# Kernel optimization log

Hardware: AMD Instinct MI355X
Metric: run time of the kernel (lower is better)

Reference implementation:

```python
import jax, jax.numpy as jnp
import numpy as np

NF = 32
B, H, W = 4, 256, 256


def conv(x, w, b, pad):
    y = jax.lax.conv_general_dilated(x, w, (1, 1), [(pad, pad), (pad, pad)],
                                     dimension_numbers=('NCHW', 'OIHW', 'NCHW'))
    return y + b[None, :, None, None]


def maxpool(x):  # kernel 3, stride 2, pad 1 (pad with -inf like torch)
    return jax.lax.reduce_window(x, -jnp.inf, jax.lax.max,
                                 (1, 1, 3, 3), (1, 1, 2, 2),
                                 [(0, 0), (0, 0), (1, 1), (1, 1)])


def up2(x):  # bilinear x2, align_corners=False (half-pixel) == jax.image default
    b, c, h, w = x.shape
    return jax.image.resize(x, (b, c, 2 * h, 2 * w), 'bilinear')


def norm_gates(g1, g2, g3):
    s = jnp.abs(g1) + jnp.abs(g2) + jnp.abs(g3)
    s = jnp.where(s == 0, 1e-6, s)
    m = (s >= 1).astype(g1.dtype)
    return tuple((1 - m) * g + m * (g / s) for g in (g1, g2, g3))


def propagate(x, g1, g2, g3, horizontal, reverse):
    """GateRecurrent2dnoind: sequential gated scan along one spatial axis.
    h[t] = (1 - g1 - g2 - g3) * x[t] + g1*h[t-1](i-1) + g2*h[t-1](i) + g3*h[t-1](i+1)
    with zero boundary for out-of-range neighbors."""
    if not horizontal:
        x, g1, g2, g3 = (jnp.swapaxes(t, 2, 3) for t in (x, g1, g2, g3))
    if reverse:
        x, g1, g2, g3 = (t[..., ::-1] for t in (x, g1, g2, g3))
    seqs = tuple(jnp.moveaxis(t, 3, 0) for t in (x, g1, g2, g3))  # [W,B,C,H]

    def step(h, inp):
        xt, a1, a2, a3 = inp
        z = jnp.zeros_like(h[..., :1])
        h_up = jnp.concatenate([z, h[..., :-1]], axis=-1)   # neighbor i-1
        h_dn = jnp.concatenate([h[..., 1:], z], axis=-1)    # neighbor i+1
        hn = (1 - a1 - a2 - a3) * xt + a1 * h_up + a2 * h + a3 * h_dn
        return hn, hn

    h0 = jnp.zeros(x.shape[:3], x.dtype)
    _, ys = jax.lax.scan(step, h0, seqs)
    out = jnp.moveaxis(ys, 0, 3)
    if reverse:
        out = out[..., ::-1]
    if not horizontal:
        out = jnp.swapaxes(out, 2, 3)
    return out


def spn_forward(x, rgb, mw, mb, c1w, c1b, c2w, c2b, c3w, c3b, c4w, c4b,
                d0w, d0b, d2w, d2b, d4w, d4b, d6w, d6b, d7w, d7b, pw, pb):
    nf = NF
    X = conv(x, mw, mb, 1)
    # VGG encoder
    f1 = conv(rgb, c1w, c1b, 1)
    p = maxpool(jax.nn.relu(f1))
    f2 = conv(p, c2w, c2b, 1)
    p = maxpool(jax.nn.relu(f2))
    f3 = conv(p, c3w, c3b, 1)
    p3 = maxpool(jax.nn.relu(f3))
    f4 = conv(p3, c4w, c4b, 1)
    # Decoder
    o = conv(f4, d0w, d0b, 0)
    o = jax.nn.elu(conv(up2(o), d2w, d2b, 1)) + f3
    o = jax.nn.elu(conv(up2(o), d4w, d4b, 1)) + f2
    o = jax.nn.elu(conv(up2(o), d6w, d6b, 1)) + f1
    guide = conv(o, d7w, d7b, 1)  # [B, 12*nf, H, W]
    G = [guide[:, i * nf:(i + 1) * nf] for i in range(12)]
    dirs = [(True, False), (True, True), (False, False), (False, True)]
    outs = []
    for k, (hor, rev) in enumerate(dirs):
        g1, g2, g3 = norm_gates(G[3 * k], G[3 * k + 1], G[3 * k + 2])
        outs.append(propagate(X, g1, g2, g3, hor, rev))
    out = jnp.maximum(jnp.maximum(outs[0], outs[1]), jnp.maximum(outs[2], outs[3]))
    return conv(out, pw, pb, 1)


def setup_inputs() -> dict:
    key = jax.random.key(0)
    ks = jax.random.split(key, 32)
    nf = NF

    def p(k, shape):
        return jax.random.normal(k, shape, dtype=jnp.float32) * 0.1

    inp = {
        'x': jax.random.normal(ks[0], (B, 3, H, W), dtype=jnp.float32),
        'rgb': jax.random.normal(ks[1], (B, 3, H, W), dtype=jnp.float32),
        'mw': p(ks[2], (nf, 3, 3, 3)), 'mb': p(ks[3], (nf,)),
        'c1w': p(ks[4], (nf, 3, 3, 3)), 'c1b': p(ks[5], (nf,)),
        'c2w': p(ks[6], (nf * 2, nf, 3, 3)), 'c2b': p(ks[7], (nf * 2,)),
        'c3w': p(ks[8], (nf * 4, nf * 2, 3, 3)), 'c3b': p(ks[9], (nf * 4,)),
        'c4w': p(ks[10], (nf * 8, nf * 4, 3, 3)), 'c4b': p(ks[11], (nf * 8,)),
        'd0w': p(ks[12], (nf * 4, nf * 8, 1, 1)), 'd0b': p(ks[13], (nf * 4,)),
        'd2w': p(ks[14], (nf * 4, nf * 4, 3, 3)), 'd2b': p(ks[15], (nf * 4,)),
        'd4w': p(ks[16], (nf * 2, nf * 4, 3, 3)), 'd4b': p(ks[17], (nf * 2,)),
        'd6w': p(ks[18], (nf, nf * 2, 3, 3)), 'd6b': p(ks[19], (nf,)),
        'd7w': p(ks[20], (nf * 12, nf, 3, 3)), 'd7b': p(ks[21], (nf * 12,)),
        'pw': p(ks[22], (3, nf, 3, 3)), 'pb': p(ks[23], (3,)),
    }
    return inp


def reference(x, rgb, mw, mb, c1w, c1b, c2w, c2b, c3w, c3b, c4w, c4b,
              d0w, d0b, d2w, d2b, d4w, d4b, d6w, d6b, d7w, d7b, pw, pb):
    return spn_forward(x, rgb, mw, mb, c1w, c1b, c2w, c2b, c3w, c3b, c4w, c4b,
                       d0w, d0b, d2w, d2b, d4w, d4b, d6w, d6b, d7w, d7b, pw, pb)
```

## Files before the change

### kernel.cpp

```cpp
#include <hip/hip_runtime.h>
#include <cstddef>
#include <cstdint>

#define DEVINL __device__ __forceinline__

typedef __attribute__((ext_vector_type(8))) _Float16 half8v;
typedef __attribute__((ext_vector_type(16))) float f32x16;

constexpr int cmax(int a, int b) { return a > b ? a : b; }


__global__ __launch_bounds__(256) void k_repack(
    const float* __restrict__ src, float* __restrict__ dst, int Cin, int Cout)
{
  int n = Cout * Cin * 9;
  int e = blockIdx.x * 256 + threadIdx.x;
  if (e >= n) return;
  int co = e / (Cin * 9);
  int r  = e - co * Cin * 9;
  int ci = r / 9;
  int k  = r - ci * 9;
  dst[(ci * 9 + k) * Cout + co] = src[e];
}

__global__ __launch_bounds__(256) void k_packwh(
    const float* __restrict__ src, _Float16* __restrict__ dst, int Cin, int Cout)
{
  int chunks = Cin >> 4;
  int total = Cout * chunks * 144;
  int e = blockIdx.x * 256 + threadIdx.x;
  if (e >= total) return;
  int n  = e / (chunks * 144);
  int r2 = e - n * chunks * 144;
  int cb = r2 / 144;
  int k  = r2 - cb * 144;
  int tap = k >> 4, ci = k & 15;
  float v = src[((size_t)n * Cin + cb * 16 + ci) * 9 + tap];
  dst[((size_t)cb * Cout + n) * 152 + k] = (_Float16)v;
}

template<int NWM, int NACC, int CHUNKS, int MODE, int GATES>
__global__ __launch_bounds__(NWM * 64) void k_convh(
    const float* __restrict__ in, const _Float16* __restrict__ wpk,
    const float* __restrict__ bias, const float* __restrict__ skip,
    void* __restrict__ outv,
    int H, int W, int wCout, int n0, int outC, int oco0)
{
  static_assert(GATES == 0 || NACC == 3, "GATES needs NACC==3");
  constexpr int NTHR = NWM * 64;
  constexpr int ROWS = NWM * 2;
  constexpr int RH = ROWS + 2;
  constexpr int N_BLK = NACC * 32;
  constexpr int MT = NWM * 32;
  constexpr int A_BYTES = RH * 18 * 16 * 2;
  constexpr int B_BYTES = N_BLK * 152 * 2;
  constexpr int MPF = MT + 1;
  constexpr int MPH = 132;
  constexpr int EP_BYTES = GATES ? (96 * MPH * 2) : (N_BLK * MPF * 4);
  constexpr int SMEM = cmax(A_BYTES + B_BYTES, EP_BYTES);

  const int tid = threadIdx.x;
  const int wave = tid >> 6, lane = tid & 63;
  const int wm = wave;
  const int tiles_x = W >> 4;
  const int tx0 = (blockIdx.x % tiles_x) << 4;
  const int ty0 = (blockIdx.x / tiles_x) * ROWS;
  const int b = blockIdx.z;
  const int nb = n0 + blockIdx.y * N_BLK;
  const int ocb = oco0 + blockIdx.y * N_BLK;

  __shared__ __align__(16) char smem[SMEM];
  _Float16* Ah = (_Float16*)smem;
  _Float16* Bh = (_Float16*)(smem + A_BYTES);

  f32x16 acc[NACC] = {};

  const size_t ps = (size_t)H * W;
  const float* inb = in + (size_t)b * (CHUNKS * 16) * ps;

  for (int cb = 0; cb < CHUNKS; ++cb) {
    __syncthreads();
    for (int e = tid; e < RH * 18; e += NTHR) {
      int r = e / 18, c = e - r * 18;
      int gy = ty0 + r - 1, gx = tx0 + c - 1;
      bool ok = (unsigned)gy < (unsigned)H && (unsigned)gx < (unsigned)W;
      const float* src = inb + (size_t)(cb * 16) * ps + (size_t)gy * W + gx;
      half8v v0, v1;
#pragma unroll
      for (int j = 0; j < 8; ++j)
        v0[j] = ok ? (_Float16)src[(size_t)j * ps] : (_Float16)0.f;
#pragma unroll
      for (int j = 0; j < 8; ++j)
        v1[j] = ok ? (_Float16)src[(size_t)(j + 8) * ps] : (_Float16)0.f;
      *(half8v*)&Ah[e * 16] = v0;
      *(half8v*)&Ah[e * 16 + 8] = v1;
    }
    {
      const _Float16* wsrc = wpk + ((size_t)cb * wCout + nb) * 152;
      for (int e = tid; e < N_BLK * 19; e += NTHR)
        *(uint4*)&Bh[e * 8] = *(const uint4*)(wsrc + e * 8);
    }
    __syncthreads();
    const int am = wm * 32 + (lane & 31);
    const int r0 = am >> 4, c0 = am & 15;
    const int kh = lane >> 5;
    const _Float16* Ab = Ah + kh * 8;
    const _Float16* Bb = Bh + kh * 8;
#pragma unroll
    for (int ks = 0; ks < 9; ++ks) {
      const int dy = ks / 3, dx = ks - dy * 3;
      half8v af = *(const half8v*)(Ab + ((r0 + dy) * 18 + (c0 + dx)) * 16);
#pragma unroll
      for (int na = 0; na < NACC; ++na) {
        const int bn = na * 32 + (lane & 31);
        half8v bf = *(const half8v*)(Bb + bn * 152 + ks * 16);
        acc[na] = __builtin_amdgcn_mfma_f32_32x32x16_f16(af, bf, acc[na], 0, 0, 0);
      }
    }
  }

  __syncthreads();

  if (GATES) {
    _Float16* EPH = (_Float16*)smem;
    const int c = lane & 31;
    const float bv0 = bias[nb + c];
    const float bv1 = bias[nb + 32 + c];
    const float bv2 = bias[nb + 64 + c];
#pragma unroll
    for (int i = 0; i < 16; ++i) {
      int m = wm * 32 + (i & 3) + 8 * (i >> 2) + 4 * (lane >> 5);
      float g1 = acc[0][i] + bv0;
      float g2 = acc[GATES ? 1 : 0][i] + bv1;
      float g3 = acc[GATES ? 2 : 0][i] + bv2;
      float s = fabsf(g1) + fabsf(g2) + fabsf(g3);
      if (s >= 1.f) { float r = 1.f / s; g1 *= r; g2 *= r; g3 *= r; }
      EPH[(size_t)(0 * 32 + c) * MPH + m] = (_Float16)g1;
      EPH[(size_t)(1 * 32 + c) * MPH + m] = (_Float16)g2;
      EPH[(size_t)(2 * 32 + c) * MPH + m] = (_Float16)g3;
    }
    __syncthreads();
    _Float16* outh = (_Float16*)outv;
    if (MODE == 2) {
      const int TOT = 96 * 16;
      for (int r = tid; r < TOT; r += NTHR) {
        int gc = r >> 4, x = r & 15;
        const _Float16* ep = EPH + (size_t)gc * MPH + x;
        _Float16 v[8];
#pragma unroll
        for (int y = 0; y < 8; ++y) v[y] = ep[y * 16];
        size_t base = ((size_t)(b * 96 + gc) * W + tx0 + x) * (size_t)H + ty0;
        *(uint4*)(outh + base) = *(const uint4*)v;
      }
    } else {
      const int TOT = 96 * ROWS;
      for (int r = tid; r < TOT; r += NTHR) {
        int gc = r / ROWS, y = r - gc * ROWS;
        const _Float16* ep = EPH + (size_t)gc * MPH + y * 16;
        _Float16 v[16];
#pragma unroll
        for (int x = 0; x < 16; ++x) v[x] = ep[x];
        size_t base = ((size_t)(b * 96 + gc) * H + ty0 + y) * (size_t)W + tx0;
        *(uint4*)(outh + base) = *(const uint4*)v;
        *(uint4*)(outh + base + 8) = *(const uint4*)(v + 8);
      }
    }
  } else {
    float* EP = (float*)smem;
    float bv[NACC];
#pragma unroll
    for (int na = 0; na < NACC; ++na) bv[na] = bias[nb + na * 32 + (lane & 31)];
#pragma unroll
    for (int na = 0; na < NACC; ++na) {
      const int c = na * 32 + (lane & 31);
#pragma unroll
      for (int i = 0; i < 16; ++i) {
        int m = wm * 32 + (i & 3) + 8 * (i >> 2) + 4 * (lane >> 5);
        EP[(size_t)c * MPF + m] = acc[na][i] + bv[na];
      }
    }
    __syncthreads();
    float* out = (float*)outv;
    const int TOT = N_BLK * ROWS;
    for (int r = tid; r < TOT; r += NTHR) {
      int c = r / ROWS, y = r - c * ROWS;
      const float* ep = EP + (size_t)c * MPF + y * 16;
      float v[16];
#pragma unroll
      for (int x = 0; x < 16; ++x) v[x] = ep[x];
      size_t base = (((size_t)b * outC + ocb + c) * H + ty0 + y) * (size_t)W + tx0;
      if (MODE == 1) {
#pragma unroll
        for (int j = 0; j < 4; ++j) {
          float4 sk = *(const float4*)(skip + base + 4 * j);
          float e0 = v[4*j+0] > 0.f ? v[4*j+0] : expm1f(v[4*j+0]);
          float e1 = v[4*j+1] > 0.f ? v[4*j+1] : expm1f(v[4*j+1]);
          float e2 = v[4*j+2] > 0.f ? v[4*j+2] : expm1f(v[4*j+2]);
          float e3 = v[4*j+3] > 0.f ? v[4*j+3] : expm1f(v[4*j+3]);
          v[4*j+0] = e0 + sk.x; v[4*j+1] = e1 + sk.y;
          v[4*j+2] = e2 + sk.z; v[4*j+3] = e3 + sk.w;
        }
      }
#pragma unroll
      for (int j = 0; j < 4; ++j)
        *(float4*)(out + base + 4 * j) = *(const float4*)(v + 4 * j);
    }
  }
}

template<int CI, int CO>
__global__ __launch_bounds__(256) void k_conv3x3f(
    const float* __restrict__ in, const float* __restrict__ wr,
    const float* __restrict__ bias, float* __restrict__ out,
    int Cin, int H, int W, int wstride, int outC)
{
  const int ntx = W >> 4;
  const int tid = threadIdx.x;
  const int tx = tid & 15, ty = tid >> 4;
  const int tx0 = (blockIdx.x % ntx) << 4, ty0 = (blockIdx.x / ntx) << 4;
  const int b = blockIdx.z;

  __shared__ float sh[CI * 324];

  float acc[CO];
#pragma unroll
  for (int co = 0; co < CO; ++co) acc[co] = bias[co];

  const float* inb = in + (size_t)b * Cin * H * W;

  for (int cb = 0; cb < Cin; cb += CI) {
    __syncthreads();
    for (int e = tid; e < CI * 324; e += 256) {
      int ci = e / 324;
      int rr = e - ci * 324;
      int r = rr / 18, c = rr - r * 18;
      int gh = ty0 + r - 1, gw = tx0 + c - 1;
      float v = 0.f;
      if ((unsigned)gh < (unsigned)H && (unsigned)gw < (unsigned)W)
        v = inb[(size_t)(cb + ci) * H * W + (size_t)gh * W + gw];
      sh[e] = v;
    }
    __syncthreads();
#pragma unroll 1
    for (int ci = 0; ci < CI; ++ci) {
      float v[9];
      const float* sp = sh + ci * 324 + ty * 18 + tx;
#pragma unroll
      for (int kh = 0; kh < 3; ++kh)
#pragma unroll
        for (int kw = 0; kw < 3; ++kw)
          v[kh * 3 + kw] = sp[kh * 18 + kw];
      const float* wp = wr + (size_t)((cb + ci) * 9) * wstride;
#pragma unroll
      for (int k = 0; k < 9; ++k)
#pragma unroll
        for (int co = 0; co < CO; ++co)
          acc[co] = fmaf(wp[(size_t)k * wstride + co], v[k], acc[co]);
    }
  }
#pragma unroll
  for (int co = 0; co < CO; ++co)
    out[(((size_t)b * outC + co) * H + ty0 + ty) * W + tx0 + tx] = acc[co];
}

__global__ __launch_bounds__(256) void k_convfin(
    const _Float16* __restrict__ om1, const _Float16* __restrict__ om2,
    const _Float16* __restrict__ omT1, const _Float16* __restrict__ omT2,
    const float* __restrict__ wr, const float* __restrict__ bias,
    float* __restrict__ out)
{
  const int H = 256, W = 256;
  const int tid = threadIdx.x;
  const int tx = tid & 15, ty = tid >> 4;
  const int tx0 = (blockIdx.x & 15) << 4, ty0 = (blockIdx.x >> 4) << 4;
  const int b = blockIdx.z;

  __shared__ float sh[32 * 324];

  for (int e = tid; e < 32 * 324; e += 256) {
    int ci = e / 324, rr = e - ci * 324;
    int r = rr / 18, c = rr - r * 18;
    int gh = ty0 + r - 1, gw = tx0 + c - 1;
    float v = 0.f;
    if ((unsigned)gh < (unsigned)H && (unsigned)gw < (unsigned)W) {
      size_t p = ((size_t)(b * 32 + ci) * H + gh) * W + gw;
      v = fmaxf((float)om1[p], (float)om2[p]);
    }
    sh[ci * 324 + r * 18 + c] = v;
  }
  __syncthreads();
  for (int e = tid; e < 32 * 324; e += 256) {
    int ci = e / 324, rr = e - ci * 324;
    int c = rr / 18, r = rr - c * 18;
    int gh = ty0 + r - 1, gw = tx0 + c - 1;
    if ((unsigned)gh < (unsigned)H && (unsigned)gw < (unsigned)W) {
      size_t p = ((size_t)(b * 32 + ci) * W + gw) * (size_t)H + gh;
      float t = fmaxf((float)omT1[p], (float)omT2[p]);
      int si = ci * 324 + r * 18 + c;
      sh[si] = fmaxf(sh[si], t);
    }
  }
  __syncthreads();

  float acc[3] = {bias[0], bias[1], bias[2]};
#pragma unroll 1
  for (int ci = 0; ci < 32; ++ci) {
    float v[9];
    const float* sp = sh + ci * 324 + ty * 18 + tx;
#pragma unroll
    for (int kh = 0; kh < 3; ++kh)
#pragma unroll
      for (int kw = 0; kw < 3; ++kw)
        v[kh * 3 + kw] = sp[kh * 18 + kw];
    const float* wp = wr + (size_t)(ci * 9) * 3;
#pragma unroll
    for (int k = 0; k < 9; ++k)
#pragma unroll
      for (int co = 0; co < 3; ++co)
        acc[co] = fmaf(wp[(size_t)k * 3 + co], v[k], acc[co]);
  }
#pragma unroll
  for (int co = 0; co < 3; ++co)
    out[(((size_t)b * 3 + co) * H + ty0 + ty) * W + tx0 + tx] = acc[co];
}

__global__ __launch_bounds__(256) void k_conv1x1(
    const float* __restrict__ in, const float* __restrict__ wgt,
    const float* __restrict__ bias, float* __restrict__ out,
    int Cin, int Cout, int H, int W)
{
  int hw = blockIdx.x * 256 + threadIdx.x;
  if (hw >= H * W) return;
  int co = blockIdx.y, b = blockIdx.z;
  const float* ip = in + (size_t)b * Cin * H * W + hw;
  const float* wp = wgt + (size_t)co * Cin;
  float acc = bias[co];
  for (int ci = 0; ci < Cin; ++ci) acc += wp[ci] * ip[(size_t)ci * H * W];
  out[((size_t)b * Cout + co) * H * W + hw] = acc;
}

__global__ __launch_bounds__(256) void k_pool(
    const float* __restrict__ in, float* __restrict__ out, int C, int H, int W)
{
  int Ho = H >> 1, Wo = W >> 1;
  int hw = blockIdx.x * 256 + threadIdx.x;
  if (hw >= Ho * Wo) return;
  int ow = hw % Wo, oh = hw / Wo;
  int c = blockIdx.y, b = blockIdx.z;
  const float* p = in + ((size_t)(b * C + c) * H) * W;
  float m = 0.f;
#pragma unroll
  for (int dh = -1; dh <= 1; ++dh) {
    int ih = 2 * oh + dh;
    if ((unsigned)ih >= (unsigned)H) continue;
    const float* r = p + (size_t)ih * W;
#pragma unroll
    for (int dw = -1; dw <= 1; ++dw) {
      int iw = 2 * ow + dw;
      if ((unsigned)iw >= (unsigned)W) continue;
      m = fmaxf(m, r[iw]);
    }
  }
  out[((size_t)(b * C + c) * Ho + oh) * Wo + ow] = m;
}

__global__ __launch_bounds__(256) void k_up2(
    const float* __restrict__ in, float* __restrict__ out, int C, int H, int W)
{
  int Ho = H * 2, Wo = W * 2;
  int hw = blockIdx.x * 256 + threadIdx.x;
  if (hw >= Ho * Wo) return;
  int ow = hw % Wo, oh = hw / Wo;
  int c = blockIdx.y, b = blockIdx.z;
  int ih = oh >> 1, iw = ow >> 1;
  int ih0, ih1, iw0, iw1; float fh0, fw0;
  if (oh & 1) { ih0 = ih; ih1 = min(ih + 1, H - 1); fh0 = 0.75f; }
  else        { ih0 = max(ih - 1, 0); ih1 = ih;     fh0 = 0.25f; }
  if (ow & 1) { iw0 = iw; iw1 = min(iw + 1, W - 1); fw0 = 0.75f; }
  else        { iw0 = max(iw - 1, 0); iw1 = iw;     fw0 = 0.25f; }
  const float* p = in + ((size_t)(b * C + c) * H) * W;
  float v = fh0 * (fw0 * p[(size_t)ih0 * W + iw0] + (1.f - fw0) * p[(size_t)ih0 * W + iw1])
          + (1.f - fh0) * (fw0 * p[(size_t)ih1 * W + iw0] + (1.f - fw0) * p[(size_t)ih1 * W + iw1]);
  out[((size_t)(b * C + c) * Ho + oh) * Wo + ow] = v;
}

__global__ void k_xcvt(const float* __restrict__ in, _Float16* __restrict__ xn,
                       _Float16* __restrict__ xt)
{
  __shared__ _Float16 t[32][33];
  int z = blockIdx.z;
  int x0 = blockIdx.x * 32, y0 = blockIdx.y * 32;
  int tx = threadIdx.x, ty = threadIdx.y;
  const float* ip = in + (size_t)z * 65536;
#pragma unroll
  for (int j = 0; j < 32; j += 8) {
    float v = ip[(size_t)(y0 + ty + j) * 256 + x0 + tx];
    xn[(size_t)z * 65536 + (size_t)(y0 + ty + j) * 256 + x0 + tx] = (_Float16)v;
    t[ty + j][tx] = (_Float16)v;
  }
  __syncthreads();
#pragma unroll
  for (int j = 0; j < 32; j += 8)
    xt[(size_t)z * 65536 + (size_t)(x0 + ty + j) * 256 + y0 + tx] = t[tx][ty + j];
}

DEVINL void gl_lds16p(const void* g, void* lds) {
  __builtin_amdgcn_global_load_lds(
      (const __attribute__((address_space(1))) unsigned int*)g,
      (__attribute__((address_space(3))) unsigned int*)lds, 16, 0, 0);
}

DEVINL float prop_step(float xv, float a1, float a2, float a3,
                       float hu, float hc, float hd) {
  return (1.f - a1 - a2 - a3) * xv + a1 * hu + a2 * hc + a3 * hd;
}

template<int REV>
DEVINL void prop_core(const _Float16* xp, const _Float16* g1,
                      const _Float16* g2, const _Float16* g3,
                      _Float16* op, int S, int P, int lane,
                      _Float16* bx, _Float16* h1, _Float16* h2, _Float16* h3,
                      _Float16* bo)
{
  float r0 = 0.f, r1 = 0.f, r2 = 0.f, r3 = 0.f;
  int cur = 0;

  auto stage = [&](int buf, int s0) {
#pragma unroll
    for (int v = 0; v < 8; ++v) {
      size_t ro = (size_t)(s0 + 2 * v) * P + lane * 8;
      gl_lds16p(xp + ro, bx + buf * 4096 + v * 512);
      gl_lds16p(g1 + ro, h1 + buf * 4096 + v * 512);
      gl_lds16p(g2 + ro, h2 + buf * 4096 + v * 512);
      gl_lds16p(g3 + ro, h3 + buf * 4096 + v * 512);
    }
  };

  stage(0, REV ? (S - 16) : 0);
  const int NT = S / 16;
  for (int t = 0; t < NT; ++t) {
    const int s0 = REV ? (S - 16 - t * 16) : (t * 16);
    asm volatile("s_waitcnt vmcnt(0)" ::: "memory");
    if (t + 1 < NT) stage(cur ^ 1, REV ? (s0 - 16) : (s0 + 16));

    for (int u = 0; u < 16; ++u) {
      const int e = REV ? (15 - u) : u;
      const _Float16* px = bx + cur * 4096 + e * 256;
      const _Float16* p1 = h1 + cur * 4096 + e * 256;
      const _Float16* p2 = h2 + cur * 4096 + e * 256;
      const _Float16* p3 = h3 + cur * 4096 + e * 256;
      float x0 = px[lane], x1 = px[lane + 64], x2 = px[lane + 128], x3 = px[lane + 192];
      float a10 = p1[lane], a11 = p1[lane + 64], a12 = p1[lane + 128], a13 = p1[lane + 192];
      float a20 = p2[lane], a21 = p2[lane + 64], a22 = p2[lane + 128], a23 = p2[lane + 192];
      float a30 = p3[lane], a31 = p3[lane + 64], a32 = p3[lane + 128], a33 = p3[lane + 192];

      float su0 = __shfl_up(r0, 1), su1 = __shfl_up(r1, 1);
      float su2 = __shfl_up(r2, 1), su3 = __shfl_up(r3, 1);
      float sd0 = __shfl_down(r0, 1), sd1 = __shfl_down(r1, 1);
      float sd2 = __shfl_down(r2, 1), sd3 = __shfl_down(r3, 1);
      float t63_0 = __shfl(r0, 63), t63_1 = __shfl(r1, 63), t63_2 = __shfl(r2, 63);
      float t0_1 = __shfl(r1, 0), t0_2 = __shfl(r2, 0), t0_3 = __shfl(r3, 0);

      float hu0 = lane ? su0 : 0.f;
      float hu1 = lane ? su1 : t63_0;
      float hu2 = lane ? su2 : t63_1;
      float hu3 = lane ? su3 : t63_2;
      float hd0 = (lane < 63) ? sd0 : t0_1;
      float hd1 = (lane < 63) ? sd1 : t0_2;
      float hd2 = (lane < 63) ? sd2 : t0_3;
      float hd3 = (lane < 63) ? sd3 : 0.f;

      r0 = prop_step(x0, a10, a20, a30, hu0, r0, hd0);
      r1 = prop_step(x1, a11, a21, a31, hu1, r1, hd1);
      r2 = prop_step(x2, a12, a22, a32, hu2, r2, hd2);
      r3 = prop_step(x3, a13, a23, a33, hu3, r3, hd3);

      _Float16* po = bo + e * 256;
      po[lane] = (_Float16)r0; po[lane + 64] = (_Float16)r1;
      po[lane + 128] = (_Float16)r2; po[lane + 192] = (_Float16)r3;
    }

    for (int j = 0; j < 16; ++j) {
      uint2 v = *(const uint2*)&bo[j * 256 + lane * 4];
      *(uint2*)(op + (size_t)(s0 + j) * P + lane * 4) = v;
    }
    cur ^= 1;
  }
}

__global__ __launch_bounds__(64) void k_prop_pair(
    const _Float16* __restrict__ Xh,
    const _Float16* __restrict__ GA, const _Float16* __restrict__ GB,
    _Float16* __restrict__ omA, _Float16* __restrict__ omB, int S, int P)
{
  const int dir = blockIdx.x >> 7;
  const int plane = blockIdx.x & 127;
  const int b = plane >> 5, c = plane & 31;
  const int lane = threadIdx.x;
  const size_t ps = (size_t)S * P;

  __shared__ __align__(16) _Float16 bx[2 * 4096];
  __shared__ __align__(16) _Float16 h1[2 * 4096];
  __shared__ __align__(16) _Float16 h2[2 * 4096];
  __shared__ __align__(16) _Float16 h3[2 * 4096];
  __shared__ __align__(16) _Float16 bo[4096];

  const _Float16* xp = Xh + (size_t)plane * ps;
  const _Float16* G = dir ? GB : GA;
  const _Float16* g1 = G + ((size_t)b * 96 + c) * ps;
  const _Float16* g2 = g1 + (size_t)32 * ps;
  const _Float16* g3 = g1 + (size_t)64 * ps;
  _Float16* op = (dir ? omB : omA) + (size_t)plane * ps;

  if (dir == 0) prop_core<0>(xp, g1, g2, g3, op, S, P, lane, bx, h1, h2, h3, bo);
  else          prop_core<1>(xp, g1, g2, g3, op, S, P, lane, bx, h1, h2, h3, bo);
}

extern "C" void kernel_launch(void* const* d_in, const int* in_sizes, int n_in,
                              void* d_out, int out_size, void* d_ws, size_t ws_size,
                              hipStream_t stream)
{
  const float* x   = (const float*)d_in[0];
  const float* rgb = (const float*)d_in[1];
  const float* mw  = (const float*)d_in[2];
  const float* mb  = (const float*)d_in[3];
  const float* c1w = (const float*)d_in[4];
  const float* c1b = (const float*)d_in[5];
  const float* c2w = (const float*)d_in[6];
  const float* c2b = (const float*)d_in[7];
  const float* c3w = (const float*)d_in[8];
  const float* c3b = (const float*)d_in[9];
  const float* c4w = (const float*)d_in[10];
  const float* c4b = (const float*)d_in[11];
  const float* d0w = (const float*)d_in[12];
  const float* d0b = (const float*)d_in[13];
  const float* d2w = (const float*)d_in[14];
  const float* d2b = (const float*)d_in[15];
  const float* d4w = (const float*)d_in[16];
  const float* d4b = (const float*)d_in[17];
  const float* d6w = (const float*)d_in[18];
  const float* d6b = (const float*)d_in[19];
  const float* d7w = (const float*)d_in[20];
  const float* d7b = (const float*)d_in[21];
  const float* pw  = (const float*)d_in[22];
  const float* pb  = (const float*)d_in[23];

  char* ws = (char*)d_ws;
  const size_t MB = 1024 * 1024;
  _Float16* Xn16 = (_Float16*)(ws + 0);
  _Float16* Xt16 = (_Float16*)(ws + 16 * MB);
  float* X32f = (float*)(ws + 32 * MB);
  float* f1   = (float*)(ws + 64 * MB);
  float* f2   = (float*)(ws + 96 * MB);
  float* f3   = (float*)(ws + 112 * MB);
  float* p1   = (float*)(ws + 120 * MB);
  float* p2   = (float*)(ws + 128 * MB);
  float* p3   = (float*)(ws + 132 * MB);
  float* f4   = (float*)(ws + 134 * MB);
  float* o0   = (float*)(ws + 138 * MB);
  float* u0   = (float*)(ws + 140 * MB);
  float* o1   = (float*)(ws + 148 * MB);
  float* u1   = (float*)(ws + 32 * MB);
  float* o2   = (float*)(ws + 160 * MB);
  float* u2   = (float*)(ws + 96 * MB);
  float* o3   = (float*)(ws + 160 * MB);
  _Float16* gbufA = (_Float16*)(ws + 32 * MB);
  _Float16* gbufB = (_Float16*)(ws + 80 * MB);
  _Float16* om1  = (_Float16*)(ws + 128 * MB);
  _Float16* om2  = (_Float16*)(ws + 144 * MB);
  _Float16* omT1 = (_Float16*)(ws + 0);
  _Float16* omT2 = (_Float16*)(ws + 160 * MB);
  char* wz = ws + 192 * MB;
  float* wmf  = (float*)wz;
  float* wc1f = wmf + 864;
  float* wpkf = wc1f + 864;
  _Float16* wc2p = (_Float16*)(wpkf + 864);
  _Float16* wc3p = wc2p + 19456;
  _Float16* wc4p = wc3p + 77824;
  _Float16* wd2p = wc4p + 311296;
  _Float16* wd4p = wd2p + 155648;
  _Float16* wd6p = wd4p + 77824;
  _Float16* wd7p = wd6p + 19456;

  hipMemsetAsync(d_ws, 0, 194 * MB, stream);

  dim3 blk(256);
  auto repf = [&](const float* s, float* d, int ci, int co) {
    int n = co * ci * 9;
    k_repack<<<dim3((n + 255) / 256), blk, 0, stream>>>(s, d, ci, co);
  };
  auto packh = [&](const float* s, _Float16* d, int ci, int co) {
    int n = co * (ci / 16) * 144;
    k_packwh<<<dim3((n + 255) / 256), blk, 0, stream>>>(s, d, ci, co);
  };
  repf(mw, wmf, 3, 32);
  repf(c1w, wc1f, 3, 32);
  repf(pw, wpkf, 32, 3);
  packh(c2w, wc2p, 32, 64);
  packh(c3w, wc3p, 64, 128);
  packh(c4w, wc4p, 128, 256);
  packh(d2w, wd2p, 128, 128);
  packh(d4w, wd4p, 128, 64);
  packh(d6w, wd6p, 64, 32);
  packh(d7w, wd7p, 32, 384);

  k_conv3x3f<3, 32><<<dim3(256, 1, 4), blk, 0, stream>>>(x, wmf, mb, X32f, 3, 256, 256, 32, 32);
  k_xcvt<<<dim3(8, 8, 128), dim3(32, 8), 0, stream>>>(X32f, Xn16, Xt16);
  k_conv3x3f<3, 32><<<dim3(256, 1, 4), blk, 0, stream>>>(rgb, wc1f, c1b, f1, 3, 256, 256, 32, 32);

  k_pool<<<dim3(64, 32, 4), blk, 0, stream>>>(f1, p1, 32, 256, 256);
  k_convh<4, 2, 2, 0, 0><<<dim3(128, 1, 4), dim3(256), 0, stream>>>(p1, wc2p, c2b, nullptr, f2, 128, 128, 64, 0, 64, 0);
  k_pool<<<dim3(16, 64, 4), blk, 0, stream>>>(f2, p2, 64, 128, 128);
  k_convh<2, 2, 4, 0, 0><<<dim3(64, 2, 4), dim3(128), 0, stream>>>(p2, wc3p, c3b, nullptr, f3, 64, 64, 128, 0, 128, 0);
  k_pool<<<dim3(4, 128, 4), blk, 0, stream>>>(f3, p3, 128, 64, 64);
  k_convh<2, 2, 8, 0, 0><<<dim3(16, 4, 4), dim3(128), 0, stream>>>(p3, wc4p, c4b, nullptr, f4, 32, 32, 256, 0, 256, 0);
  k_conv1x1<<<dim3(4, 128, 4), blk, 0, stream>>>(f4, d0w, d0b, o0, 256, 128, 32, 32);

  k_up2<<<dim3(16, 128, 4), blk, 0, stream>>>(o0, u0, 128, 32, 32);
  k_convh<2, 2, 8, 1, 0><<<dim3(64, 2, 4), dim3(128), 0, stream>>>(u0, wd2p, d2b, f3, o1, 64, 64, 128, 0, 128, 0);
  k_up2<<<dim3(64, 128, 4), blk, 0, stream>>>(o1, u1, 128, 64, 64);
  k_convh<4, 2, 8, 1, 0><<<dim3(128, 1, 4), dim3(256), 0, stream>>>(u1, wd4p, d4b, f2, o2, 128, 128, 64, 0, 64, 0);
  k_up2<<<dim3(256, 64, 4), blk, 0, stream>>>(o2, u2, 64, 128, 128);
  k_convh<4, 1, 4, 1, 0><<<dim3(512, 1, 4), dim3(256), 0, stream>>>(u2, wd6p, d6b, f1, o3, 256, 256, 32, 0, 32, 0);

  k_convh<4, 3, 2, 0, 1><<<dim3(512, 1, 4), dim3(256), 0, stream>>>(o3, wd7p, d7b, nullptr, gbufA, 256, 256, 384, 192, 96, 0);
  k_convh<4, 3, 2, 0, 1><<<dim3(512, 1, 4), dim3(256), 0, stream>>>(o3, wd7p, d7b, nullptr, gbufB, 256, 256, 384, 288, 96, 0);
  k_prop_pair<<<dim3(256), dim3(64), 0, stream>>>(Xn16, gbufA, gbufB, om1, om2, 256, 256);

  k_convh<4, 3, 2, 2, 1><<<dim3(512, 1, 4), dim3(256), 0, stream>>>(o3, wd7p, d7b, nullptr, gbufA, 256, 256, 384, 0, 96, 0);
  k_convh<4, 3, 2, 2, 1><<<dim3(512, 1, 4), dim3(256), 0, stream>>>(o3, wd7p, d7b, nullptr, gbufB, 256, 256, 384, 96, 96, 0);
  k_prop_pair<<<dim3(256), dim3(64), 0, stream>>>(Xt16, gbufA, gbufB, omT1, omT2, 256, 256);

  k_convfin<<<dim3(256, 1, 4), blk, 0, stream>>>(om1, om2, omT1, omT2, wpkf, pb, (float*)d_out);
}
```

Baseline: 972.6 us.

## Assign contiguous 4-element spans per lane in gated propagation scan

Changes the scan's lane-to-row mapping so each lane owns four adjacent positions instead of four strided ones. Neighbor terms now come mostly from registers, which cuts cross-lane shuffles from 14 to 2 per step. LDS reads become one 8-byte vector load per operand, and results go straight to global memory, dropping the LDS output staging buffer and its copy loop. The inner loop is also fully unrolled; the cost is many small per-step global stores.

```diff
diff --git a/kernel.cpp b/kernel.cpp
--- a/kernel.cpp
+++ b/kernel.cpp
@@ -5,6 +5,7 @@
 #define DEVINL __device__ __forceinline__
 
 typedef __attribute__((ext_vector_type(8))) _Float16 half8v;
+typedef __attribute__((ext_vector_type(4))) _Float16 half4v;
 typedef __attribute__((ext_vector_type(16))) float f32x16;
 
 constexpr int cmax(int a, int b) { return a > b ? a : b; }
@@ -410,17 +411,11 @@
       (__attribute__((address_space(3))) unsigned int*)lds, 16, 0, 0);
 }
 
-DEVINL float prop_step(float xv, float a1, float a2, float a3,
-                       float hu, float hc, float hd) {
-  return (1.f - a1 - a2 - a3) * xv + a1 * hu + a2 * hc + a3 * hd;
-}
-
 template<int REV>
 DEVINL void prop_core(const _Float16* xp, const _Float16* g1,
                       const _Float16* g2, const _Float16* g3,
                       _Float16* op, int S, int P, int lane,
-                      _Float16* bx, _Float16* h1, _Float16* h2, _Float16* h3,
-                      _Float16* bo)
+                      _Float16* bx, _Float16* h1, _Float16* h2, _Float16* h3)
 {
   float r0 = 0.f, r1 = 0.f, r2 = 0.f, r3 = 0.f;
   int cur = 0;
@@ -443,46 +438,33 @@
     asm volatile("s_waitcnt vmcnt(0)" ::: "memory");
     if (t + 1 < NT) stage(cur ^ 1, REV ? (s0 - 16) : (s0 + 16));
 
+#pragma unroll
     for (int u = 0; u < 16; ++u) {
       const int e = REV ? (15 - u) : u;
-      const _Float16* px = bx + cur * 4096 + e * 256;
-      const _Float16* p1 = h1 + cur * 4096 + e * 256;
-      const _Float16* p2 = h2 + cur * 4096 + e * 256;
-      const _Float16* p3 = h3 + cur * 4096 + e * 256;
-      float x0 = px[lane], x1 = px[lane + 64], x2 = px[lane + 128], x3 = px[lane + 192];
-      float a10 = p1[lane], a11 = p1[lane + 64], a12 = p1[lane + 128], a13 = p1[lane + 192];
-      float a20 = p2[lane], a21 = p2[lane + 64], a22 = p2[lane + 128], a23 = p2[lane + 192];
-      float a30 = p3[lane], a31 = p3[lane + 64], a32 = p3[lane + 128], a33 = p3[lane + 192];
-
-      float su0 = __shfl_up(r0, 1), su1 = __shfl_up(r1, 1);
-      float su2 = __shfl_up(r2, 1), su3 = __shfl_up(r3, 1);
-      float sd0 = __shfl_down(r0, 1), sd1 = __shfl_down(r1, 1);
-      float sd2 = __shfl_down(r2, 1), sd3 = __shfl_down(r3, 1);
-      float t63_0 = __shfl(r0, 63), t63_1 = __shfl(r1, 63), t63_2 = __shfl(r2, 63);
-      float t0_1 = __shfl(r1, 0), t0_2 = __shfl(r2, 0), t0_3 = __shfl(r3, 0);
-
-      float hu0 = lane ? su0 : 0.f;
-      float hu1 = lane ? su1 : t63_0;
-      float hu2 = lane ? su2 : t63_1;
-      float hu3 = lane ? su3 : t63_2;
-      float hd0 = (lane < 63) ? sd0 : t0_1;
-      float hd1 = (lane < 63) ? sd1 : t0_2;
-      float hd2 = (lane < 63) ? sd2 : t0_3;
-      float hd3 = (lane < 63) ? sd3 : 0.f;
-
-      r0 = prop_step(x0, a10, a20, a30, hu0, r0, hd0);
-      r1 = prop_step(x1, a11, a21, a31, hu1, r1, hd1);
-      r2 = prop_step(x2, a12, a22, a32, hu2, r2, hd2);
-      r3 = prop_step(x3, a13, a23, a33, hu3, r3, hd3);
-
-      _Float16* po = bo + e * 256;
-      po[lane] = (_Float16)r0; po[lane + 64] = (_Float16)r1;
-      po[lane + 128] = (_Float16)r2; po[lane + 192] = (_Float16)r3;
-    }
-
-    for (int j = 0; j < 16; ++j) {
-      uint2 v = *(const uint2*)&bo[j * 256 + lane * 4];
-      *(uint2*)(op + (size_t)(s0 + j) * P + lane * 4) = v;
+      half4v xv = *(const half4v*)(bx + cur * 4096 + e * 256 + 4 * lane);
+      half4v a1 = *(const half4v*)(h1 + cur * 4096 + e * 256 + 4 * lane);
+      half4v a2 = *(const half4v*)(h2 + cur * 4096 + e * 256 + 4 * lane);
+      half4v a3 = *(const half4v*)(h3 + cur * 4096 + e * 256 + 4 * lane);
+
+      float hu0 = __shfl_up(r3, 1);
+      float hd3 = __shfl_down(r0, 1);
+      if (lane == 0)  hu0 = 0.f;
+      if (lane == 63) hd3 = 0.f;
+
+      float o0 = r0, o1 = r1, o2 = r2, o3v = r3;
+      float x0 = xv[0], x1 = xv[1], x2 = xv[2], x3 = xv[3];
+      float a10 = a1[0], a11 = a1[1], a12 = a1[2], a13 = a1[3];
+      float a20 = a2[0], a21 = a2[1], a22 = a2[2], a23 = a2[3];
+      float a30 = a3[0], a31 = a3[1], a32 = a3[2], a33 = a3[3];
+
+      r0 = (1.f - a10 - a20 - a30) * x0 + a10 * hu0 + a20 * o0 + a30 * o1;
+      r1 = (1.f - a11 - a21 - a31) * x1 + a11 * o0  + a21 * o1 + a31 * o2;
+      r2 = (1.f - a12 - a22 - a32) * x2 + a12 * o1  + a22 * o2 + a32 * o3v;
+      r3 = (1.f - a13 - a23 - a33) * x3 + a13 * o2  + a23 * o3v + a33 * hd3;
+
+      half4v hv; hv[0] = (_Float16)r0; hv[1] = (_Float16)r1;
+      hv[2] = (_Float16)r2; hv[3] = (_Float16)r3;
+      *(half4v*)(op + (size_t)(s0 + e) * P + 4 * lane) = hv;
     }
     cur ^= 1;
   }
@@ -503,7 +485,6 @@
   __shared__ __align__(16) _Float16 h1[2 * 4096];
   __shared__ __align__(16) _Float16 h2[2 * 4096];
   __shared__ __align__(16) _Float16 h3[2 * 4096];
-  __shared__ __align__(16) _Float16 bo[4096];
 
   const _Float16* xp = Xh + (size_t)plane * ps;
   const _Float16* G = dir ? GB : GA;
@@ -512,8 +493,8 @@
   const _Float16* g3 = g1 + (size_t)64 * ps;
   _Float16* op = (dir ? omB : omA) + (size_t)plane * ps;
 
-  if (dir == 0) prop_core<0>(xp, g1, g2, g3, op, S, P, lane, bx, h1, h2, h3, bo);
-  else          prop_core<1>(xp, g1, g2, g3, op, S, P, lane, bx, h1, h2, h3, bo);
+  if (dir == 0) prop_core<0>(xp, g1, g2, g3, op, S, P, lane, bx, h1, h2, h3);
+  else          prop_core<1>(xp, g1, g2, g3, op, S, P, lane, bx, h1, h2, h3);
 }
 
 extern "C" void kernel_launch(void* const* d_in, const int* in_sizes, int n_in,
```

New measurement: 934.9 us. 1.04x faster.
